# Optimization experiments

Hardware: AMD Instinct MI355X
Metric: run time of the kernel (lower is better)

## Reference

```python
import jax, jax.numpy as jnp
import numpy as np

MODEL_SIZE = 1024
H = 16
KEY_SIZE = MODEL_SIZE // H


def setup_inputs() -> dict:
    key = jax.random.key(0)
    ks = jax.random.split(key, 10)
    B, SQ, SK, D = 2, 2048, 2048, MODEL_SIZE
    s = 1.0 / np.sqrt(D)
    return {
        "decoder_output": jax.random.normal(ks[0], (B, SQ, D), jnp.float32),
        "encoder_output": jax.random.normal(ks[1], (B, SK, D), jnp.float32),
        "wq": jax.random.normal(ks[2], (D, D), jnp.float32) * s,
        "bq": jnp.zeros((D,), jnp.float32),
        "wk": jax.random.normal(ks[3], (D, D), jnp.float32) * s,
        "bk": jnp.zeros((D,), jnp.float32),
        "wv": jax.random.normal(ks[4], (D, D), jnp.float32) * s,
        "bv": jnp.zeros((D,), jnp.float32),
        "wo": jax.random.normal(ks[5], (D, D), jnp.float32) * s,
        "bo": jnp.zeros((D,), jnp.float32),
    }


def reference(decoder_output, encoder_output, wq, bq, wk, bk, wv, bv, wo, bo):
    B, SQ, D = decoder_output.shape
    SK = encoder_output.shape[1]
    # QKV projections (Dense = x @ W + b)
    q = decoder_output @ wq + bq          # [B, SQ, D]
    k = encoder_output @ wk + bk          # [B, SK, D]
    v = encoder_output @ wv + bv          # [B, SK, D]
    # split heads -> [B, H, S, key_size]
    q = q.reshape(B, SQ, H, KEY_SIZE).transpose(0, 2, 1, 3)
    k = k.reshape(B, SK, H, KEY_SIZE).transpose(0, 2, 1, 3)
    v = v.reshape(B, SK, H, KEY_SIZE).transpose(0, 2, 1, 3)
    scale = 1.0 / jnp.sqrt(jnp.asarray(KEY_SIZE, q.dtype))
    score = jnp.einsum('bhqd,bhkd->bhqk', q, k) * scale   # [B, H, SQ, SK]
    align = jax.nn.softmax(score, axis=-1)
    ctx = jnp.einsum('bhqk,bhkd->bhqd', align, v)          # [B, H, SQ, key_size]
    ctx = ctx.transpose(0, 2, 1, 3).reshape(B, SQ, D)
    return ctx @ wo + bo
```

## Files before the change

### kernel.cpp

```cpp
#include <hip/hip_runtime.h>
#include <hip/hip_fp16.h>

typedef __attribute__((ext_vector_type(8))) _Float16 f16x8;
typedef __attribute__((ext_vector_type(4))) _Float16 f16x4;
typedef __attribute__((ext_vector_type(4))) float    f32x4;

#define MFMA_F16(a,b,c) __builtin_amdgcn_mfma_f32_16x16x32_f16((a),(b),(c),0,0,0)
#define GL16(s_, d_) __builtin_amdgcn_global_load_lds((const __attribute__((address_space(1))) void*)(s_), \
                       (__attribute__((address_space(3))) void*)(d_), 16, 0, 0)


__global__ __launch_bounds__(256) void k_cast(const float* __restrict__ dec, const float* __restrict__ enc,
                                              _Float16* __restrict__ dd, _Float16* __restrict__ de)
{
  int i = blockIdx.x * 256 + threadIdx.x;
  float4 a = ((const float4*)dec)[i];
  float4 b = ((const float4*)enc)[i];
  f16x4 ha = {(_Float16)a.x, (_Float16)a.y, (_Float16)a.z, (_Float16)a.w};
  f16x4 hb = {(_Float16)b.x, (_Float16)b.y, (_Float16)b.z, (_Float16)b.w};
  ((f16x4*)dd)[i] = ha;
  ((f16x4*)de)[i] = hb;
}

__global__ __launch_bounds__(256) void k_wt(const float* __restrict__ wq, const float* __restrict__ wk,
                                            const float* __restrict__ wv, const float* __restrict__ wo,
                                            _Float16* __restrict__ dst0)
{
  __shared__ float tile[32][33];
  int z = blockIdx.z;
  const float* w = (z==0)?wq:(z==1)?wk:(z==2)?wv:wo;
  _Float16* dst = dst0 + (size_t)z * (1024u*1024u);
  int tx = threadIdx.x, ty = threadIdx.y;
  int n0 = blockIdx.x*32, k0 = blockIdx.y*32;
#pragma unroll
  for (int r = 0; r < 4; ++r)
    tile[ty + 8*r][tx] = w[(size_t)(k0 + ty + 8*r)*1024 + n0 + tx];
  __syncthreads();
#pragma unroll
  for (int r = 0; r < 4; ++r)
    dst[(size_t)(n0 + ty + 8*r)*1024 + k0 + tx] = (_Float16)tile[tx][ty + 8*r];
}

__device__ __forceinline__ void gemm_core_128(const _Float16* __restrict__ A, const _Float16* __restrict__ BT,
                                              int m0, int n0, _Float16* lds, f32x4 acc[4][4])
{
  const int t    = threadIdx.x;
  const int lane = t & 63;
  const int wid  = t >> 6;
  const int lr   = lane & 15, lg = lane >> 4;
  const int wm   = (wid & 1) * 64, wn = (wid >> 1) * 64;
  const int swz  = (lr >> 2) & 3;

  const int cm0 = t >> 2,         ck0 = (((t      ) & 3) ^ (((t      ) >> 4) & 3)) * 8;
  const int cm1 = (t + 256) >> 2, ck1 = (((t + 256) & 3) ^ (((t + 256) >> 4) & 3)) * 8;
  const _Float16* Arow0 = A  + (size_t)(m0 + cm0) * 1024 + ck0;
  const _Float16* Arow1 = A  + (size_t)(m0 + cm1) * 1024 + ck1;
  const _Float16* Brow0 = BT + (size_t)(n0 + cm0) * 1024 + ck0;
  const _Float16* Brow1 = BT + (size_t)(n0 + cm1) * 1024 + ck1;

  _Float16* l0 = lds + t*8;
  _Float16* l1 = lds + (t+256)*8;
  _Float16* l2 = lds + 4096 + t*8;
  _Float16* l3 = lds + 4096 + (t+256)*8;

#define STAGE_GL(buf_, ko_) { GL16(Arow0+(ko_), l0+(buf_)*8192); GL16(Arow1+(ko_), l1+(buf_)*8192); \
                              GL16(Brow0+(ko_), l2+(buf_)*8192); GL16(Brow1+(ko_), l3+(buf_)*8192); }

  int aoff[4], boff[4];
#pragma unroll
  for (int s = 0; s < 4; ++s) {
    aoff[s] = (wm + s*16 + lr)*32 + ((lg ^ swz) << 3);
    boff[s] = (wn + s*16 + lr)*32 + ((lg ^ swz) << 3);
  }

  const f32x4 z4 = {0.f,0.f,0.f,0.f};
#pragma unroll
  for (int i = 0; i < 4; ++i)
#pragma unroll
    for (int j = 0; j < 4; ++j) acc[i][j] = z4;

  STAGE_GL(0, 0);
  STAGE_GL(1, 32);

  int cur = 0;
#pragma unroll 1
  for (int kt = 0; kt < 32; ++kt) {
    if (kt < 31) { asm volatile("s_waitcnt vmcnt(4)" ::: "memory"); }
    else         { asm volatile("s_waitcnt vmcnt(0)" ::: "memory"); }
    __builtin_amdgcn_s_barrier();
    __builtin_amdgcn_sched_barrier(0);
    const _Float16* la = lds + cur * 8192;
    const _Float16* lb = la + 4096;
    f16x8 af[4], bf[4];
#pragma unroll
    for (int s = 0; s < 4; ++s) af[s] = *(const f16x8*)(la + aoff[s]);
#pragma unroll
    for (int s = 0; s < 4; ++s) bf[s] = *(const f16x8*)(lb + boff[s]);
#pragma unroll
    for (int i = 0; i < 4; ++i)
#pragma unroll
      for (int j = 0; j < 4; ++j)
        acc[i][j] = MFMA_F16(af[i], bf[j], acc[i][j]);
    if (kt < 30) {
      int nx = cur + 2; if (nx >= 3) nx -= 3;
      STAGE_GL(nx, (kt + 2) * 32);
    }
    cur = (cur + 1 == 3) ? 0 : cur + 1;
  }
#undef STAGE_GL
}

__global__ __launch_bounds__(256, 3) void k_qkv(const _Float16* __restrict__ dec16, const _Float16* __restrict__ enc16,
                                                const _Float16* __restrict__ wT,
                                                const float* __restrict__ bq, const float* __restrict__ bk,
                                                const float* __restrict__ bv,
                                                _Float16* __restrict__ Qo, _Float16* __restrict__ Ko,
                                                _Float16* __restrict__ Vt)
{
  __shared__ _Float16 lds[24576];
  const int lin = blockIdx.x;
  const int b768 = (lin & 7) * 96 + (lin >> 3);
  const int z  = b768 >> 8;
  const int bx = b768 & 255;
  const _Float16* A    = (z == 0) ? dec16 : enc16;
  const _Float16* BT   = wT + (size_t)z * (1024u*1024u);
  const float*    bias = (z == 0) ? bq : (z == 1) ? bk : bv;

  const int m0 = (bx >> 3) * 128, n0 = (bx & 7) * 128;
  const int lane = threadIdx.x & 63, wid = threadIdx.x >> 6;
  const int lr = lane & 15, lg = lane >> 4;
  const int wm = (wid & 1) * 64, wn = (wid >> 1) * 64;
  const float QSCL = 0.125f * 1.44269504f;

  f32x4 acc[4][4];
  gemm_core_128(A, BT, m0, n0, lds, acc);

  if (z < 2) {
    _Float16* dst = (z == 0) ? Qo : Ko;
    const float scl = (z == 0) ? QSCL : 1.0f;
#pragma unroll
    for (int i = 0; i < 4; ++i)
#pragma unroll
      for (int j = 0; j < 4; ++j) {
        int n = n0 + wn + j*16 + lr;
        int h = n >> 6, d = n & 63;
        float bb = bias[n];
        f32x4 v = acc[i][j];
#pragma unroll
        for (int r = 0; r < 4; ++r) {
          int m = m0 + wm + i*16 + 4*lg + r;
          int b = m >> 11, s = m & 2047;
          dst[((size_t)(b*16 + h)*2048 + s)*64 + d] = (_Float16)((v[r] + bb) * scl);
        }
      }
  } else {
#pragma unroll
    for (int i = 0; i < 4; ++i)
#pragma unroll
      for (int j = 0; j < 4; ++j) {
        int n = n0 + wn + j*16 + lr;
        int h = n >> 6, d = n & 63;
        float bb = bias[n];
        int m = m0 + wm + i*16 + 4*lg;
        int b = m >> 11, s = m & 2047;
        int sp = (s & ~31) | (((s >> 2) & 3) << 3) | (((s >> 4) & 1) << 2);
        f16x4 pv = {(_Float16)(acc[i][j][0] + bb), (_Float16)(acc[i][j][1] + bb),
                    (_Float16)(acc[i][j][2] + bb), (_Float16)(acc[i][j][3] + bb)};
        *(f16x4*)&Vt[((size_t)(b*16 + h)*64 + d)*2048 + sp] = pv;
      }
  }
}

__global__ __launch_bounds__(256, 3) void k_out(const _Float16* __restrict__ ctx, const _Float16* __restrict__ woT,
                                                const float* __restrict__ bo, float* __restrict__ out)
{
  __shared__ _Float16 lds[24576];
  const int lin = blockIdx.x;
  const int bx = (lin & 7) * 32 + (lin >> 3);
  const int m0 = (bx >> 3) * 128, n0 = (bx & 7) * 128;
  const int lane = threadIdx.x & 63, wid = threadIdx.x >> 6;
  const int lr = lane & 15, lg = lane >> 4;
  const int wm = (wid & 1) * 64, wn = (wid >> 1) * 64;

  f32x4 acc[4][4];
  gemm_core_128(ctx, woT, m0, n0, lds, acc);

#pragma unroll
  for (int i = 0; i < 4; ++i)
#pragma unroll
    for (int j = 0; j < 4; ++j) {
      int n = n0 + wn + j*16 + lr;
      float bb = bo[n];
#pragma unroll
      for (int r = 0; r < 4; ++r) {
        int m = m0 + wm + i*16 + 4*lg + r;
        out[(size_t)m*1024 + n] = acc[i][j][r] + bb;
      }
    }
}

__global__ __launch_bounds__(256, 2) void k_attn(const _Float16* __restrict__ Q, const _Float16* __restrict__ K,
                                                 const _Float16* __restrict__ Vt, _Float16* __restrict__ ctx)
{
  __shared__ _Float16 lds[16384];
  const int bid  = blockIdx.x;
  const int xcd  = bid & 7, slot = bid >> 3;
  const int bh   = xcd*4 + (slot >> 4);
  const int qt   = slot & 15;
  const int t    = threadIdx.x;
  const int wid  = t >> 6, lane = t & 63;
  const int lr   = lane & 15, lg = lane >> 4;
  const int qbase = qt*128 + wid*32;

  const _Float16* Qp = Q  + ((size_t)bh*2048 + qbase)*64;
  const _Float16* Kp = K  + (size_t)bh*2048*64;
  const _Float16* Vp = Vt + (size_t)bh*64*2048;

  const f32x4 z4 = {0.f,0.f,0.f,0.f};

  const int c1  = t + 256;
  const int kr0 = t  >> 3, lc0 = ((t  & 7) ^ (kr0 & 7)) * 8;
  const int kr1 = c1 >> 3, lc1 = ((c1 & 7) ^ (kr1 & 7)) * 8;
  const _Float16* Ks0 = Kp + (size_t)kr0*64   + lc0;
  const _Float16* Ks1 = Kp + (size_t)kr1*64   + lc1;
  const _Float16* Vs0 = Vp + (size_t)kr0*2048 + lc0;
  const _Float16* Vs1 = Vp + (size_t)kr1*2048 + lc1;
  _Float16* lK0 = lds + t*8;
  _Float16* lK1 = lds + c1*8;
  _Float16* lV0 = lds + 4096 + t*8;
  _Float16* lV1 = lds + 4096 + c1*8;

#define STAGE(buf_, kt_) { GL16(Ks0 + (size_t)(kt_)*4096, lK0 + (buf_)*8192); \
                           GL16(Ks1 + (size_t)(kt_)*4096, lK1 + (buf_)*8192); \
                           GL16(Vs0 + (kt_)*64,           lV0 + (buf_)*8192); \
                           GL16(Vs1 + (kt_)*64,           lV1 + (buf_)*8192); }

  f16x8 qf[2][2];
#pragma unroll
  for (int qs = 0; qs < 2; ++qs)
#pragma unroll
    for (int d2 = 0; d2 < 2; ++d2)
      qf[qs][d2] = *(const f16x8*)&Qp[(size_t)(qs*16 + lr)*64 + d2*32 + 8*lg];

  f32x4 acc[4][2];
#pragma unroll
  for (int dt = 0; dt < 4; ++dt) { acc[dt][0] = z4; acc[dt][1] = z4; }
  float lrun[2] = {0.f, 0.f};

  const int kswz = lr & 7;

  STAGE(0, 0);
  __syncthreads();

  int cur = 0;
#pragma unroll 1
  for (int kt = 0; kt < 32; ++kt) {
    if (kt < 31) STAGE(cur ^ 1, kt + 1);
    const _Float16* bK = lds + cur*8192;
    const _Float16* bV = bK + 4096;
#pragma unroll
    for (int ks2 = 0; ks2 < 2; ++ks2) {
      f16x8 kf[2][2], vf[4];
#pragma unroll
      for (int ks = 0; ks < 2; ++ks)
#pragma unroll
        for (int d2 = 0; d2 < 2; ++d2)
          kf[ks][d2] = *(const f16x8*)&bK[(ks2*32 + ks*16 + lr)*64 + ((((d2<<2)|lg) ^ kswz) << 3)];
#pragma unroll
      for (int dt = 0; dt < 4; ++dt)
        vf[dt] = *(const f16x8*)&bV[(dt*16 + lr)*64 + ((((ks2<<2)|lg) ^ kswz) << 3)];

      f32x4 st[2][2];
      __builtin_amdgcn_s_setprio(1);
#pragma unroll
      for (int ks = 0; ks < 2; ++ks)
#pragma unroll
        for (int qs = 0; qs < 2; ++qs) {
          f32x4 s_ = MFMA_F16(kf[ks][0], qf[qs][0], z4);
          st[ks][qs] = MFMA_F16(kf[ks][1], qf[qs][1], s_);
        }
      __builtin_amdgcn_s_setprio(0);
      f16x8 pt[2];
#pragma unroll
      for (int qs = 0; qs < 2; ++qs) {
        float pv[8];
#pragma unroll
        for (int i = 0; i < 4; ++i) { pv[i] = st[0][qs][i]; pv[4+i] = st[1][qs][i]; }
        float ssum = 0.f;
        f16x8 ptv;
#pragma unroll
        for (int i = 0; i < 8; ++i) {
          float e = exp2f(pv[i]);
          ssum += e;
          ptv[i] = (_Float16)e;
        }
        lrun[qs] += ssum;
        pt[qs] = ptv;
      }
      __builtin_amdgcn_s_setprio(1);
#pragma unroll
      for (int dt = 0; dt < 4; ++dt)
#pragma unroll
        for (int qs = 0; qs < 2; ++qs)
          acc[dt][qs] = MFMA_F16(vf[dt], pt[qs], acc[dt][qs]);
      __builtin_amdgcn_s_setprio(0);
    }
    __syncthreads();
    cur ^= 1;
  }

#pragma unroll
  for (int qs = 0; qs < 2; ++qs) {
    float L = lrun[qs];
    L += __shfl_xor(L, 16);
    L += __shfl_xor(L, 32);
    float inv = 1.f / L;
    int q = qbase + qs*16 + lr;
    _Float16* cp = ctx + ((size_t)((bh >> 4)*2048 + q))*1024 + (bh & 15)*64;
#pragma unroll
    for (int dt = 0; dt < 4; ++dt) {
      f16x4 o = {(_Float16)(acc[dt][qs][0]*inv), (_Float16)(acc[dt][qs][1]*inv),
                 (_Float16)(acc[dt][qs][2]*inv), (_Float16)(acc[dt][qs][3]*inv)};
      *(f16x4*)&cp[dt*16 + 4*lg] = o;
    }
  }
#undef STAGE
}

extern "C" void kernel_launch(void* const* d_in, const int* in_sizes, int n_in,
                              void* d_out, int out_size, void* d_ws, size_t ws_size,
                              hipStream_t stream) {
  const float* dec = (const float*)d_in[0];
  const float* enc = (const float*)d_in[1];
  const float* wq  = (const float*)d_in[2];
  const float* bq  = (const float*)d_in[3];
  const float* wk  = (const float*)d_in[4];
  const float* bk  = (const float*)d_in[5];
  const float* wv  = (const float*)d_in[6];
  const float* bv  = (const float*)d_in[7];
  const float* wo  = (const float*)d_in[8];
  const float* bo  = (const float*)d_in[9];

  char* ws = (char*)d_ws;
  _Float16* dec16 = (_Float16*)(ws + (0ull  << 20));
  _Float16* enc16 = (_Float16*)(ws + (8ull  << 20));
  _Float16* wT    = (_Float16*)(ws + (16ull << 20));
  _Float16* Qh    = (_Float16*)(ws + (24ull << 20));
  _Float16* Kh    = (_Float16*)(ws + (32ull << 20));
  _Float16* Vt    = (_Float16*)(ws + (40ull << 20));
  _Float16* ctx   = (_Float16*)(ws + (48ull << 20));
  float* out = (float*)d_out;

  k_cast<<<4096, 256, 0, stream>>>(dec, enc, dec16, enc16);
  k_wt<<<dim3(32, 32, 4), dim3(32, 8), 0, stream>>>(wq, wk, wv, wo, wT);
  k_qkv<<<768, 256, 0, stream>>>(dec16, enc16, wT, bq, bk, bv, Qh, Kh, Vt);
  k_attn<<<512, 256, 0, stream>>>(Qh, Kh, Vt, ctx);
  k_out<<<256, 256, 0, stream>>>(ctx, wT + 3ull*1024*1024, bo, out);
}
```

Before: 211.1 us.

## Halve attention and output-projection tiles to double grid size and occupancy

The attention kernel now gives each wave 16 query rows instead of 32, doubling the grid to 1024 blocks and raising launch bounds to 4 blocks per CU. The output projection replaces the shared 128x128 GEMM core with a dedicated 64x128 tile kernel using a 3-stage LDS ring with explicit vmcnt waits, doubling its grid to 512 blocks. The aim is to fill all CUs on the 256-CU part and cut tail effects. The cost is that K/V tiles are reloaded twice as often per query, and each K/V fragment read from LDS feeds half as many MFMAs.

Measured after the change: 220.4 us. +4.4%, slower.

```diff
diff --git a/kernel.cpp b/kernel.cpp
--- a/kernel.cpp
+++ b/kernel.cpp
@@ -174,19 +174,74 @@
 __global__ __launch_bounds__(256, 3) void k_out(const _Float16* __restrict__ ctx, const _Float16* __restrict__ woT,
                                                 const float* __restrict__ bo, float* __restrict__ out)
 {
-  __shared__ _Float16 lds[24576];
+  __shared__ _Float16 lds[18432];
   const int lin = blockIdx.x;
-  const int bx = (lin & 7) * 32 + (lin >> 3);
-  const int m0 = (bx >> 3) * 128, n0 = (bx & 7) * 128;
-  const int lane = threadIdx.x & 63, wid = threadIdx.x >> 6;
+  const int bx  = (lin & 7) * 64 + (lin >> 3);
+  const int m0 = (bx >> 3) * 64, n0 = (bx & 7) * 128;
+  const int t    = threadIdx.x;
+  const int lane = t & 63, wid = t >> 6;
   const int lr = lane & 15, lg = lane >> 4;
-  const int wm = (wid & 1) * 64, wn = (wid >> 1) * 64;
-
-  f32x4 acc[4][4];
-  gemm_core_128(ctx, woT, m0, n0, lds, acc);
-
-#pragma unroll
-  for (int i = 0; i < 4; ++i)
+  const int wm = (wid & 1) * 32, wn = (wid >> 1) * 64;
+  const int swz = (lr >> 2) & 3;
+
+  const int cm0 = t >> 2,         ck0 = (((t      ) & 3) ^ (((t      ) >> 4) & 3)) * 8;
+  const int cm1 = (t + 256) >> 2, ck1 = (((t + 256) & 3) ^ (((t + 256) >> 4) & 3)) * 8;
+  const _Float16* Arow  = ctx + (size_t)(m0 + cm0) * 1024 + ck0;
+  const _Float16* Brow0 = woT + (size_t)(n0 + cm0) * 1024 + ck0;
+  const _Float16* Brow1 = woT + (size_t)(n0 + cm1) * 1024 + ck1;
+
+  _Float16* lA  = lds + t*8;
+  _Float16* lB0 = lds + 2048 + t*8;
+  _Float16* lB1 = lds + 2048 + (t+256)*8;
+
+#define STAGE_O(buf_, ko_) { GL16(Arow+(ko_),  lA +(buf_)*6144); \
+                             GL16(Brow0+(ko_), lB0+(buf_)*6144); \
+                             GL16(Brow1+(ko_), lB1+(buf_)*6144); }
+
+  int aoff[2], boff[4];
+#pragma unroll
+  for (int i = 0; i < 2; ++i) aoff[i] = (wm + i*16 + lr)*32 + ((lg ^ swz) << 3);
+#pragma unroll
+  for (int j = 0; j < 4; ++j) boff[j] = 2048 + (wn + j*16 + lr)*32 + ((lg ^ swz) << 3);
+
+  const f32x4 z4 = {0.f,0.f,0.f,0.f};
+  f32x4 acc[2][4];
+#pragma unroll
+  for (int i = 0; i < 2; ++i)
+#pragma unroll
+    for (int j = 0; j < 4; ++j) acc[i][j] = z4;
+
+  STAGE_O(0, 0);
+  STAGE_O(1, 32);
+
+  int cur = 0;
+#pragma unroll 1
+  for (int kt = 0; kt < 32; ++kt) {
+    if (kt < 31) { asm volatile("s_waitcnt vmcnt(3)" ::: "memory"); }
+    else         { asm volatile("s_waitcnt vmcnt(0)" ::: "memory"); }
+    __builtin_amdgcn_s_barrier();
+    __builtin_amdgcn_sched_barrier(0);
+    const _Float16* lb = lds + cur * 6144;
+    f16x8 af[2], bf[4];
+#pragma unroll
+    for (int i = 0; i < 2; ++i) af[i] = *(const f16x8*)(lb + aoff[i]);
+#pragma unroll
+    for (int j = 0; j < 4; ++j) bf[j] = *(const f16x8*)(lb + boff[j]);
+#pragma unroll
+    for (int i = 0; i < 2; ++i)
+#pragma unroll
+      for (int j = 0; j < 4; ++j)
+        acc[i][j] = MFMA_F16(af[i], bf[j], acc[i][j]);
+    if (kt < 30) {
+      int nx = cur + 2; if (nx >= 3) nx -= 3;
+      STAGE_O(nx, (kt + 2) * 32);
+    }
+    cur = (cur + 1 == 3) ? 0 : cur + 1;
+  }
+#undef STAGE_O
+
+#pragma unroll
+  for (int i = 0; i < 2; ++i)
 #pragma unroll
     for (int j = 0; j < 4; ++j) {
       int n = n0 + wn + j*16 + lr;
@@ -199,18 +254,18 @@
     }
 }
 
-__global__ __launch_bounds__(256, 2) void k_attn(const _Float16* __restrict__ Q, const _Float16* __restrict__ K,
+__global__ __launch_bounds__(256, 4) void k_attn(const _Float16* __restrict__ Q, const _Float16* __restrict__ K,
                                                  const _Float16* __restrict__ Vt, _Float16* __restrict__ ctx)
 {
   __shared__ _Float16 lds[16384];
   const int bid  = blockIdx.x;
   const int xcd  = bid & 7, slot = bid >> 3;
-  const int bh   = xcd*4 + (slot >> 4);
-  const int qt   = slot & 15;
+  const int bh   = xcd*4 + (slot >> 5);
+  const int qt   = slot & 31;
   const int t    = threadIdx.x;
   const int wid  = t >> 6, lane = t & 63;
   const int lr   = lane & 15, lg = lane >> 4;
-  const int qbase = qt*128 + wid*32;
+  const int qbase = qt*64 + wid*16;
 
   const _Float16* Qp = Q  + ((size_t)bh*2048 + qbase)*64;
   const _Float16* Kp = K  + (size_t)bh*2048*64;
@@ -235,17 +290,15 @@
                            GL16(Vs0 + (kt_)*64,           lV0 + (buf_)*8192); \
                            GL16(Vs1 + (kt_)*64,           lV1 + (buf_)*8192); }
 
-  f16x8 qf[2][2];
-#pragma unroll
-  for (int qs = 0; qs < 2; ++qs)
-#pragma unroll
-    for (int d2 = 0; d2 < 2; ++d2)
-      qf[qs][d2] = *(const f16x8*)&Qp[(size_t)(qs*16 + lr)*64 + d2*32 + 8*lg];
-
-  f32x4 acc[4][2];
-#pragma unroll
-  for (int dt = 0; dt < 4; ++dt) { acc[dt][0] = z4; acc[dt][1] = z4; }
-  float lrun[2] = {0.f, 0.f};
+  f16x8 qf[2];
+#pragma unroll
+  for (int d2 = 0; d2 < 2; ++d2)
+    qf[d2] = *(const f16x8*)&Qp[(size_t)lr*64 + d2*32 + 8*lg];
+
+  f32x4 acc[4];
+#pragma unroll
+  for (int dt = 0; dt < 4; ++dt) acc[dt] = z4;
+  float lrun = 0.f;
 
   const int kswz = lr & 7;
 
@@ -270,59 +323,47 @@
       for (int dt = 0; dt < 4; ++dt)
         vf[dt] = *(const f16x8*)&bV[(dt*16 + lr)*64 + ((((ks2<<2)|lg) ^ kswz) << 3)];
 
-      f32x4 st[2][2];
+      f32x4 st[2];
       __builtin_amdgcn_s_setprio(1);
 #pragma unroll
-      for (int ks = 0; ks < 2; ++ks)
-#pragma unroll
-        for (int qs = 0; qs < 2; ++qs) {
-          f32x4 s_ = MFMA_F16(kf[ks][0], qf[qs][0], z4);
-          st[ks][qs] = MFMA_F16(kf[ks][1], qf[qs][1], s_);
-        }
+      for (int ks = 0; ks < 2; ++ks) {
+        f32x4 s_ = MFMA_F16(kf[ks][0], qf[0], z4);
+        st[ks] = MFMA_F16(kf[ks][1], qf[1], s_);
+      }
       __builtin_amdgcn_s_setprio(0);
-      f16x8 pt[2];
-#pragma unroll
-      for (int qs = 0; qs < 2; ++qs) {
-        float pv[8];
-#pragma unroll
-        for (int i = 0; i < 4; ++i) { pv[i] = st[0][qs][i]; pv[4+i] = st[1][qs][i]; }
-        float ssum = 0.f;
-        f16x8 ptv;
-#pragma unroll
-        for (int i = 0; i < 8; ++i) {
-          float e = exp2f(pv[i]);
-          ssum += e;
-          ptv[i] = (_Float16)e;
-        }
-        lrun[qs] += ssum;
-        pt[qs] = ptv;
+      float pv[8];
+#pragma unroll
+      for (int i = 0; i < 4; ++i) { pv[i] = st[0][i]; pv[4+i] = st[1][i]; }
+      float ssum = 0.f;
+      f16x8 ptv;
+#pragma unroll
+      for (int i = 0; i < 8; ++i) {
+        float e = exp2f(pv[i]);
+        ssum += e;
+        ptv[i] = (_Float16)e;
       }
+      lrun += ssum;
       __builtin_amdgcn_s_setprio(1);
 #pragma unroll
       for (int dt = 0; dt < 4; ++dt)
-#pragma unroll
-        for (int qs = 0; qs < 2; ++qs)
-          acc[dt][qs] = MFMA_F16(vf[dt], pt[qs], acc[dt][qs]);
+        acc[dt] = MFMA_F16(vf[dt], ptv, acc[dt]);
       __builtin_amdgcn_s_setprio(0);
     }
     __syncthreads();
     cur ^= 1;
   }
 
-#pragma unroll
-  for (int qs = 0; qs < 2; ++qs) {
-    float L = lrun[qs];
-    L += __shfl_xor(L, 16);
-    L += __shfl_xor(L, 32);
-    float inv = 1.f / L;
-    int q = qbase + qs*16 + lr;
-    _Float16* cp = ctx + ((size_t)((bh >> 4)*2048 + q))*1024 + (bh & 15)*64;
-#pragma unroll
-    for (int dt = 0; dt < 4; ++dt) {
-      f16x4 o = {(_Float16)(acc[dt][qs][0]*inv), (_Float16)(acc[dt][qs][1]*inv),
-                 (_Float16)(acc[dt][qs][2]*inv), (_Float16)(acc[dt][qs][3]*inv)};
-      *(f16x4*)&cp[dt*16 + 4*lg] = o;
-    }
+  float L = lrun;
+  L += __shfl_xor(L, 16);
+  L += __shfl_xor(L, 32);
+  float inv = 1.f / L;
+  int q = qbase + lr;
+  _Float16* cp = ctx + ((size_t)((bh >> 4)*2048 + q))*1024 + (bh & 15)*64;
+#pragma unroll
+  for (int dt = 0; dt < 4; ++dt) {
+    f16x4 o = {(_Float16)(acc[dt][0]*inv), (_Float16)(acc[dt][1]*inv),
+               (_Float16)(acc[dt][2]*inv), (_Float16)(acc[dt][3]*inv)};
+    *(f16x4*)&cp[dt*16 + 4*lg] = o;
   }
 #undef STAGE
 }
@@ -354,6 +395,6 @@
   k_cast<<<4096, 256, 0, stream>>>(dec, enc, dec16, enc16);
   k_wt<<<dim3(32, 32, 4), dim3(32, 8), 0, stream>>>(wq, wk, wv, wo, wT);
   k_qkv<<<768, 256, 0, stream>>>(dec16, enc16, wT, bq, bk, bv, Qh, Kh, Vt);
-  k_attn<<<512, 256, 0, stream>>>(Qh, Kh, Vt, ctx);
-  k_out<<<256, 256, 0, stream>>>(ctx, wT + 3ull*1024*1024, bo, out);
-}
+  k_attn<<<1024, 256, 0, stream>>>(Qh, Kh, Vt, ctx);
+  k_out<<<512, 256, 0, stream>>>(ctx, wT + 3ull*1024*1024, bo, out);
+}
```
